# Kernel tuning notes

Measured on AMD Instinct MI355X. Metric: run time of the kernel, lower is better.

Reference implementation:

```python
import jax, jax.numpy as jnp
import numpy as np

N_NODES = 20000
HEADS = 4


def _gat_conv(x, src, dst, W, att_src, att_dst, bias, concat):
    # PyG GATConv: h = x @ W -> [N, H, C]; edge score = leaky_relu(a_s[src]+a_d[dst], 0.2);
    # segment softmax over dst; scatter-add weighted messages.
    N = x.shape[0]
    H, C = att_src.shape[1], att_src.shape[2]
    h = (x @ W).reshape(N, H, C)
    a_s = jnp.sum(h * att_src, axis=-1)  # [N, H]
    a_d = jnp.sum(h * att_dst, axis=-1)  # [N, H]
    e = jax.nn.leaky_relu(a_s[src] + a_d[dst], negative_slope=0.2)  # [E, H]
    m = jax.ops.segment_max(e, dst, num_segments=N)  # [N, H]
    e = jnp.exp(e - m[dst])
    denom = jax.ops.segment_sum(e, dst, num_segments=N)
    alpha = e / (denom[dst] + 1e-16)  # [E, H]
    msg = h[src] * alpha[:, :, None]  # [E, H, C]
    out = jax.ops.segment_sum(msg, dst, num_segments=N)  # [N, H, C]
    if concat:
        out = out.reshape(N, H * C)
    else:
        out = out.mean(axis=1)
    return out + bias


def setup_inputs() -> dict:
    key = jax.random.key(0)
    ks = jax.random.split(key, 16)
    N, F_in, Hd, H, Z = N_NODES, 256, 128, HEADS, 64
    E = 320000
    x = jax.random.normal(ks[0], (N, F_in), dtype=jnp.float32)
    edge_index = jax.random.randint(ks[1], (2, E), 0, N, dtype=jnp.int64)
    def xavier(k, shape):
        fan_in, fan_out = shape[0], shape[1]
        lim = float(np.sqrt(6.0 / (fan_in + fan_out)))
        return jax.random.uniform(k, shape, jnp.float32, -lim, lim)
    inp = {"x": x, "edge_index": edge_index}
    dims = [(F_in, Hd), (Hd * H, Hd), (Hd * H, Hd)]
    for i, (din, dout) in enumerate(dims, 1):
        inp[f"W{i}"] = xavier(ks[2 * i], (din, H * dout))
        inp[f"att{i}_src"] = jax.random.normal(ks[2 * i + 1], (1, H, dout), dtype=jnp.float32) * 0.1
        inp[f"att{i}_dst"] = jax.random.normal(jax.random.fold_in(ks[2 * i + 1], 7), (1, H, dout), dtype=jnp.float32) * 0.1
        bdim = H * dout if i < 3 else dout
        inp[f"b{i}"] = jnp.zeros((bdim,), dtype=jnp.float32)
    inp["fc_W"] = xavier(ks[10], (Hd, 2 * Z))
    inp["fc_b"] = jnp.zeros((2 * Z,), dtype=jnp.float32)
    return inp


def reference(x, edge_index, W1, att1_src, att1_dst, b1, W2, att2_src, att2_dst, b2,
              W3, att3_src, att3_dst, b3, fc_W, fc_b):
    N = x.shape[0]
    # add_self_loops=True (PyG default)
    loop = jnp.arange(N, dtype=edge_index.dtype)
    src = jnp.concatenate([edge_index[0], loop])
    dst = jnp.concatenate([edge_index[1], loop])
    h = jax.nn.leaky_relu(_gat_conv(x, src, dst, W1, att1_src, att1_dst, b1, True), 0.01)
    h = jax.nn.leaky_relu(_gat_conv(h, src, dst, W2, att2_src, att2_dst, b2, True), 0.01)
    h = _gat_conv(h, src, dst, W3, att3_src, att3_dst, b3, False)
    z = h @ fc_W + fc_b
    mu, logvar = jnp.split(z, 2, axis=1)
    return (mu, jnp.exp(logvar))
```

## Files before the change

kernel.cpp:

```cpp
#include <hip/hip_runtime.h>
#include <hip/hip_bf16.h>

typedef unsigned short u16;
typedef unsigned int u32;
typedef __attribute__((ext_vector_type(8))) short bf16x8;
typedef __attribute__((ext_vector_type(4))) float f32x4;
typedef __attribute__((ext_vector_type(8))) u16 u16x8;
typedef __attribute__((ext_vector_type(4))) u16 u16x4;

#define NN 20000
#define NE 320000
#define HC 512

__device__ __forceinline__ float bf2f(u16 u){ return __uint_as_float(((u32)u)<<16); }
__device__ __forceinline__ u16 f2bf(float x){
  __hip_bfloat16 h = __float2bfloat16(x);
  return *reinterpret_cast<u16*>(&h);
}
__device__ __forceinline__ float escore(float x){
  float e = x > 0.f ? x : 0.2f*x;
  return __expf(fminf(e, 80.f));
}

typedef const __attribute__((address_space(1))) unsigned int* gas_t;
typedef __attribute__((address_space(3))) unsigned int* las_t;
__device__ __forceinline__ void gl16(const void* g, void* l){
  __builtin_amdgcn_global_load_lds((gas_t)g, (las_t)l, 16, 0, 0);
}

__global__ __launch_bounds__(256) void cast_kernel(const float* __restrict__ in, u16* __restrict__ out, int total){
  int i = (blockIdx.x*256 + threadIdx.x)*4;
  if (i >= total) return;
  float4 v = *(const float4*)(in + i);
  u16x4 o = { f2bf(v.x), f2bf(v.y), f2bf(v.z), f2bf(v.w) };
  *(u16x4*)(out + i) = o;
}

__global__ __launch_bounds__(256) void transpose_cast(const float* __restrict__ W, u16* __restrict__ WT,
                                                      int K, int N){
  __shared__ u16 t[32][33];
  int bx = blockIdx.x*32;
  int by = blockIdx.y*32;
  int tx = threadIdx.x & 31, ty = threadIdx.x >> 5;
  for (int r = ty; r < 32; r += 8) t[r][tx] = f2bf(W[(size_t)(by+r)*N + bx + tx]);
  __syncthreads();
  for (int r = ty; r < 32; r += 8) WT[(size_t)(bx+r)*K + by + tx] = t[tx][r];
}

__global__ void detect_kernel(const int* __restrict__ ei, int* __restrict__ flag){
  __shared__ int nz;
  if (threadIdx.x == 0) nz = 0;
  __syncthreads();
  int c = 0;
  for (int k = threadIdx.x; k < 4096; k += 256) if (ei[2*k + 1] != 0) c++;
  atomicAdd(&nz, c);
  __syncthreads();
  if (threadIdx.x == 0) *flag = (nz == 0) ? 1 : 0;
}

__global__ __launch_bounds__(256) void normalize_edges(const int* __restrict__ ei, const int* __restrict__ flag,
    int* __restrict__ src, int* __restrict__ dst, int E){
  int e = blockIdx.x*256 + threadIdx.x;
  if (e >= E) return;
  if (*flag){ src[e] = ei[2*e]; dst[e] = ei[2*(E + e)]; }
  else      { src[e] = ei[e];   dst[e] = ei[E + e]; }
}

__global__ __launch_bounds__(256) void gemm_bf16(const u16* __restrict__ A, const u16* __restrict__ BT,
                                                 u16* __restrict__ C, int M, int K){
  __shared__ __align__(16) u16 Ads[128][64];
  __shared__ __align__(16) u16 Bds[128][64];
  const int bm = blockIdx.x, bn = blockIdx.y;
  const int tid = threadIdx.x;
  const int lane = tid & 63, wid = tid >> 6;
  const int wr = (wid >> 1) << 6, wc = (wid & 1) << 6;
  f32x4 acc[4][4] = {};
  const int row0 = bm*128;
  const int wbase = tid & 192;
  for (int k0 = 0; k0 < K; k0 += 64){
    #pragma unroll
    for (int p = 0; p < 4; ++p){
      int idx = p*256 + tid;
      int r = idx >> 3, cg = idx & 7;
      int csg = cg ^ (r & 7);
      int gr = row0 + r; if (gr >= M) gr = M - 1;
      gl16(A + (size_t)gr*K + k0 + csg*8, (u16*)Ads + (size_t)(p*256 + wbase)*8);
      gl16(BT + (size_t)(bn*128 + r)*K + k0 + csg*8, (u16*)Bds + (size_t)(p*256 + wbase)*8);
    }
    __syncthreads();
    #pragma unroll
    for (int kk = 0; kk < 64; kk += 32){
      const int lr = lane & 15;
      const int lk = kk + ((lane >> 4) << 3);
      bf16x8 a[4], b[4];
      #pragma unroll
      for (int i = 0; i < 4; ++i){
        int ar = wr + 16*i + lr;
        a[i] = *(const bf16x8*)&Ads[ar][lk ^ ((ar & 7) << 3)];
      }
      #pragma unroll
      for (int j = 0; j < 4; ++j){
        int br = wc + 16*j + lr;
        b[j] = *(const bf16x8*)&Bds[br][lk ^ ((br & 7) << 3)];
      }
      #pragma unroll
      for (int i = 0; i < 4; ++i)
        #pragma unroll
        for (int j = 0; j < 4; ++j)
          acc[i][j] = __builtin_amdgcn_mfma_f32_16x16x32_bf16(a[i], b[j], acc[i][j], 0, 0, 0);
    }
    __syncthreads();
  }
  const int lr = lane & 15, r4 = (lane >> 4) << 2;
  #pragma unroll
  for (int i = 0; i < 4; ++i)
    #pragma unroll
    for (int j = 0; j < 4; ++j){
      int col = bn*128 + wc + 16*j + lr;
      #pragma unroll
      for (int r = 0; r < 4; ++r){
        int row = row0 + wr + 16*i + r4 + r;
        if (row < M) C[(size_t)row*HC + col] = f2bf(acc[i][j][r]);
      }
    }
}

__global__ __launch_bounds__(256) void asad_kernel(const u16* __restrict__ h,
    const float* __restrict__ attS, const float* __restrict__ attD,
    float* __restrict__ a_s, float* __restrict__ a_d, int N){
  int wid = blockIdx.x*4 + (threadIdx.x >> 6);
  if (wid >= N) return;
  int lane = threadIdx.x & 63;
  u16x8 v = *(const u16x8*)(h + (size_t)wid*HC + lane*8);
  float4 s0 = *(const float4*)(attS + lane*8);
  float4 s1 = *(const float4*)(attS + lane*8 + 4);
  float4 d0 = *(const float4*)(attD + lane*8);
  float4 d1 = *(const float4*)(attD + lane*8 + 4);
  float sv[8] = {s0.x,s0.y,s0.z,s0.w,s1.x,s1.y,s1.z,s1.w};
  float dv[8] = {d0.x,d0.y,d0.z,d0.w,d1.x,d1.y,d1.z,d1.w};
  float ps = 0.f, pd = 0.f;
  #pragma unroll
  for (int t = 0; t < 8; ++t){ float hv = bf2f(v[t]); ps += hv*sv[t]; pd += hv*dv[t]; }
  #pragma unroll
  for (int off = 1; off < 16; off <<= 1){
    ps += __shfl_xor(ps, off, 64);
    pd += __shfl_xor(pd, off, 64);
  }
  if ((lane & 15) == 0){
    int hh = lane >> 4;
    a_s[wid*4 + hh] = ps;
    a_d[wid*4 + hh] = pd;
  }
}

__global__ __launch_bounds__(256) void hist_kernel(const int* __restrict__ dst, int* __restrict__ cnt, int E){
  int e = blockIdx.x*256 + threadIdx.x;
  if (e < E) atomicAdd(&cnt[dst[e]], 1);
}

__global__ __launch_bounds__(1024) void scan_kernel(const int* __restrict__ cnt,
    int* __restrict__ offs, int* __restrict__ cur, int N){
  __shared__ int bsum[1024];
  int tid = threadIdx.x;
  const int CH = (N + 1023) >> 10;
  int lo = tid*CH, hi = min(lo + CH, N);
  int s = 0;
  for (int i = lo; i < hi; ++i) s += cnt[i];
  bsum[tid] = s;
  __syncthreads();
  for (int off = 1; off < 1024; off <<= 1){
    int t = (tid >= off) ? bsum[tid - off] : 0;
    __syncthreads();
    bsum[tid] += t;
    __syncthreads();
  }
  int run = (tid > 0) ? bsum[tid - 1] : 0;
  for (int i = lo; i < hi; ++i){
    offs[i] = run; cur[i] = run; run += cnt[i];
  }
  if (tid == 1023) offs[N] = bsum[1023];
}

__global__ __launch_bounds__(256) void scatter_kernel(const int* __restrict__ src, const int* __restrict__ dst,
    int* __restrict__ cur, int* __restrict__ src_sorted, int E){
  int e = blockIdx.x*256 + threadIdx.x;
  if (e >= E) return;
  int d = dst[e];
  int pos = atomicAdd(&cur[d], 1);
  src_sorted[pos] = src[e];
}

template<int MODE>
__global__ __launch_bounds__(256) void agg_kernel(const u16* __restrict__ h,
    const int* __restrict__ srcs, const int* __restrict__ offs,
    const float* __restrict__ a_s, const float* __restrict__ a_d,
    const float* __restrict__ bias, void* __restrict__ outp, int N){
  int d = blockIdx.x*4 + (threadIdx.x >> 6);
  if (d >= N) return;
  int lane = threadIdx.x & 63;
  int head = lane >> 4;
  float adv = a_d[d*4 + head];
  float acc[8];
  float dsum;
  {
    float w = escore(a_s[d*4 + head] + adv);
    dsum = w;
    u16x8 v = *(const u16x8*)(h + (size_t)d*HC + lane*8);
    #pragma unroll
    for (int t = 0; t < 8; ++t) acc[t] = w*bf2f(v[t]);
  }
  int p0 = offs[d], p1 = offs[d+1];
  int p = p0;
  for (; p + 3 < p1; p += 4){
    int s0 = srcs[p], s1 = srcs[p+1], s2 = srcs[p+2], s3 = srcs[p+3];
    float w0 = escore(a_s[s0*4 + head] + adv);
    float w1 = escore(a_s[s1*4 + head] + adv);
    float w2 = escore(a_s[s2*4 + head] + adv);
    float w3 = escore(a_s[s3*4 + head] + adv);
    u16x8 v0 = *(const u16x8*)(h + (size_t)s0*HC + lane*8);
    u16x8 v1 = *(const u16x8*)(h + (size_t)s1*HC + lane*8);
    u16x8 v2 = *(const u16x8*)(h + (size_t)s2*HC + lane*8);
    u16x8 v3 = *(const u16x8*)(h + (size_t)s3*HC + lane*8);
    dsum += w0 + w1 + w2 + w3;
    #pragma unroll
    for (int t = 0; t < 8; ++t)
      acc[t] += w0*bf2f(v0[t]) + w1*bf2f(v1[t]) + w2*bf2f(v2[t]) + w3*bf2f(v3[t]);
  }
  for (; p < p1; ++p){
    int s = srcs[p];
    float w = escore(a_s[s*4 + head] + adv);
    u16x8 v = *(const u16x8*)(h + (size_t)s*HC + lane*8);
    dsum += w;
    #pragma unroll
    for (int t = 0; t < 8; ++t) acc[t] += w*bf2f(v[t]);
  }
  float inv = 1.0f / (dsum + 1e-16f);
  if (MODE < 2){
    u16* act = (u16*)outp;
    u16x8 o;
    #pragma unroll
    for (int t = 0; t < 8; ++t){
      float x = acc[t]*inv + bias[lane*8 + t];
      x = x > 0.f ? x : 0.01f*x;
      o[t] = f2bf(x);
    }
    *(u16x8*)(act + (size_t)d*HC + lane*8) = o;
  } else {
    #pragma unroll
    for (int t = 0; t < 8; ++t){
      acc[t] *= inv;
      acc[t] += __shfl_xor(acc[t], 16, 64);
      acc[t] += __shfl_xor(acc[t], 32, 64);
    }
    if (lane < 16){
      float* hf = (float*)outp;
      int c0 = lane*8;
      float4 o0 = {0.25f*acc[0] + bias[c0+0], 0.25f*acc[1] + bias[c0+1],
                   0.25f*acc[2] + bias[c0+2], 0.25f*acc[3] + bias[c0+3]};
      float4 o1 = {0.25f*acc[4] + bias[c0+4], 0.25f*acc[5] + bias[c0+5],
                   0.25f*acc[6] + bias[c0+6], 0.25f*acc[7] + bias[c0+7]};
      *(float4*)(hf + (size_t)d*128 + c0)     = o0;
      *(float4*)(hf + (size_t)d*128 + c0 + 4) = o1;
    }
  }
}

__global__ __launch_bounds__(256) void hsplit_kernel(const float* __restrict__ hfin,
    u16* __restrict__ Hhi, u16* __restrict__ Hlo, int total){
  int i = (blockIdx.x*256 + threadIdx.x)*4;
  if (i >= total) return;
  float4 v = *(const float4*)(hfin + i);
  float r[4] = {v.x, v.y, v.z, v.w};
  u16x4 hi, lo;
  #pragma unroll
  for (int t = 0; t < 4; ++t){
    hi[t] = f2bf(r[t]);
    lo[t] = f2bf(r[t] - bf2f(hi[t]));
  }
  *(u16x4*)(Hhi + i) = hi;
  *(u16x4*)(Hlo + i) = lo;
}

__global__ __launch_bounds__(256) void wsplit_kernel(const float* __restrict__ W,
    u16* __restrict__ WThi, u16* __restrict__ WTlo){
  int i = blockIdx.x*256 + threadIdx.x;
  int k = i >> 7, o = i & 127;
  float w = W[i];
  u16 hi = f2bf(w);
  u16 lo = f2bf(w - bf2f(hi));
  WThi[o*128 + k] = hi;
  WTlo[o*128 + k] = lo;
}

__global__ __launch_bounds__(256) void fc_mfma(const u16* __restrict__ Hhi, const u16* __restrict__ Hlo,
    const u16* __restrict__ WThi, const u16* __restrict__ WTlo,
    const float* __restrict__ fcb, float* __restrict__ outp, int M){
  __shared__ __align__(16) u16 Ahi[128][64];
  __shared__ __align__(16) u16 Alo[128][64];
  __shared__ __align__(16) u16 Bhi[128][64];
  __shared__ __align__(16) u16 Blo[128][64];
  const int tid = threadIdx.x;
  const int lane = tid & 63, wid = tid >> 6;
  const int wr = (wid >> 1) << 6, wc = (wid & 1) << 6;
  f32x4 acc[4][4] = {};
  const int row0 = blockIdx.x*128;
  for (int k0 = 0; k0 < 128; k0 += 64){
    #pragma unroll
    for (int p = 0; p < 4; ++p){
      int idx = p*256 + tid;
      int r = idx >> 3;
      int c = (idx & 7) << 3;
      int cs = c ^ ((r & 7) << 3);
      int gr = row0 + r; if (gr >= M) gr = M - 1;
      *(u16x8*)&Ahi[r][cs] = *(const u16x8*)(Hhi + (size_t)gr*128 + k0 + c);
      *(u16x8*)&Alo[r][cs] = *(const u16x8*)(Hlo + (size_t)gr*128 + k0 + c);
      *(u16x8*)&Bhi[r][cs] = *(const u16x8*)(WThi + (size_t)r*128 + k0 + c);
      *(u16x8*)&Blo[r][cs] = *(const u16x8*)(WTlo + (size_t)r*128 + k0 + c);
    }
    __syncthreads();
    #pragma unroll
    for (int kk = 0; kk < 64; kk += 32){
      const int lr = lane & 15;
      const int lk = kk + ((lane >> 4) << 3);
      bf16x8 ah[4], al[4], bh[4], bl[4];
      #pragma unroll
      for (int i = 0; i < 4; ++i){
        int ar = wr + 16*i + lr;
        int sw = lk ^ ((ar & 7) << 3);
        ah[i] = *(const bf16x8*)&Ahi[ar][sw];
        al[i] = *(const bf16x8*)&Alo[ar][sw];
      }
      #pragma unroll
      for (int j = 0; j < 4; ++j){
        int br = wc + 16*j + lr;
        int sw = lk ^ ((br & 7) << 3);
        bh[j] = *(const bf16x8*)&Bhi[br][sw];
        bl[j] = *(const bf16x8*)&Blo[br][sw];
      }
      #pragma unroll
      for (int i = 0; i < 4; ++i)
        #pragma unroll
        for (int j = 0; j < 4; ++j){
          acc[i][j] = __builtin_amdgcn_mfma_f32_16x16x32_bf16(ah[i], bh[j], acc[i][j], 0, 0, 0);
          acc[i][j] = __builtin_amdgcn_mfma_f32_16x16x32_bf16(ah[i], bl[j], acc[i][j], 0, 0, 0);
          acc[i][j] = __builtin_amdgcn_mfma_f32_16x16x32_bf16(al[i], bh[j], acc[i][j], 0, 0, 0);
        }
    }
    __syncthreads();
  }
  const int lr = lane & 15, r4 = (lane >> 4) << 2;
  #pragma unroll
  for (int i = 0; i < 4; ++i)
    #pragma unroll
    for (int j = 0; j < 4; ++j){
      int o = wc + 16*j + lr;
      float bb = fcb[o];
      #pragma unroll
      for (int r = 0; r < 4; ++r){
        int row = row0 + wr + 16*i + r4 + r;
        if (row < M){
          float z = acc[i][j][r] + bb;
          if (o < 64) outp[(size_t)row*64 + o] = z;
          else        outp[(size_t)M*64 + (size_t)row*64 + (o - 64)] = expf(z);
        }
      }
    }
}

extern "C" void kernel_launch(void* const* d_in, const int* in_sizes, int n_in,
                              void* d_out, int out_size, void* d_ws, size_t ws_size,
                              hipStream_t stream){
  const float* x    = (const float*)d_in[0];
  const int* ei     = (const int*)d_in[1];
  const float* W1   = (const float*)d_in[2];
  const float* att1s= (const float*)d_in[3];
  const float* att1d= (const float*)d_in[4];
  const float* b1   = (const float*)d_in[5];
  const float* W2   = (const float*)d_in[6];
  const float* att2s= (const float*)d_in[7];
  const float* att2d= (const float*)d_in[8];
  const float* b2   = (const float*)d_in[9];
  const float* W3   = (const float*)d_in[10];
  const float* att3s= (const float*)d_in[11];
  const float* att3d= (const float*)d_in[12];
  const float* b3   = (const float*)d_in[13];
  const float* fcW  = (const float*)d_in[14];
  const float* fcb  = (const float*)d_in[15];
  float* outp = (float*)d_out;

  char* ws = (char*)d_ws;
  size_t off = 0;
  auto alloc = [&](size_t bytes) -> void* {
    void* p = ws + off;
    off = (off + bytes + 255) & ~(size_t)255;
    return p;
  };
  u16*   xb     = (u16*)  alloc((size_t)NN*256*2);
  u16*   h      = (u16*)  alloc((size_t)NN*HC*2);
  u16*   act    = (u16*)  alloc((size_t)NN*HC*2);
  float* hfin   = (float*)alloc((size_t)NN*128*4);
  u16*   Hhi    = (u16*)  alloc((size_t)NN*128*2);
  u16*   Hlo    = (u16*)  alloc((size_t)NN*128*2);
  float* a_s    = (float*)alloc((size_t)NN*4*4);
  float* a_d    = (float*)alloc((size_t)NN*4*4);
  int*   cnt    = (int*)  alloc((size_t)NN*4);
  int*   cur    = (int*)  alloc((size_t)NN*4);
  int*   offs   = (int*)  alloc((size_t)(NN+1)*4);
  int*   src32  = (int*)  alloc((size_t)NE*4);
  int*   dst32  = (int*)  alloc((size_t)NE*4);
  int*   srcs   = (int*)  alloc((size_t)NE*4);
  u16*   WT1    = (u16*)  alloc((size_t)512*256*2);
  u16*   WT2    = (u16*)  alloc((size_t)512*512*2);
  u16*   WT3    = (u16*)  alloc((size_t)512*512*2);
  u16*   WThi   = (u16*)  alloc((size_t)128*128*2);
  u16*   WTlo   = (u16*)  alloc((size_t)128*128*2);
  int*   flag   = (int*)  alloc(256);

  cast_kernel<<<5000, 256, 0, stream>>>(x, xb, NN*256);
  transpose_cast<<<dim3(16, 8),  256, 0, stream>>>(W1, WT1, 256, 512);
  transpose_cast<<<dim3(16, 16), 256, 0, stream>>>(W2, WT2, 512, 512);
  transpose_cast<<<dim3(16, 16), 256, 0, stream>>>(W3, WT3, 512, 512);
  wsplit_kernel<<<64, 256, 0, stream>>>(fcW, WThi, WTlo);

  detect_kernel<<<1, 256, 0, stream>>>(ei, flag);
  normalize_edges<<<1250, 256, 0, stream>>>(ei, flag, src32, dst32, NE);

  hipMemsetAsync(cnt, 0, (size_t)NN*4, stream);
  hist_kernel<<<1250, 256, 0, stream>>>(dst32, cnt, NE);
  scan_kernel<<<1, 1024, 0, stream>>>(cnt, offs, cur, NN);
  scatter_kernel<<<1250, 256, 0, stream>>>(src32, dst32, cur, srcs, NE);

  const float* attS[3] = {att1s, att2s, att3s};
  const float* attD[3] = {att1d, att2d, att3d};
  const u16*   WT[3]   = {WT1, WT2, WT3};
  const int    Kd[3]   = {256, 512, 512};

  for (int layer = 0; layer < 3; ++layer){
    const u16* Ain = (layer == 0) ? xb : act;
    gemm_bf16<<<dim3(157, 4), 256, 0, stream>>>(Ain, WT[layer], h, NN, Kd[layer]);
    asad_kernel<<<5000, 256, 0, stream>>>(h, attS[layer], attD[layer], a_s, a_d, NN);
    if (layer == 0)
      agg_kernel<0><<<5000, 256, 0, stream>>>(h, srcs, offs, a_s, a_d, b1, act, NN);
    else if (layer == 1)
      agg_kernel<1><<<5000, 256, 0, stream>>>(h, srcs, offs, a_s, a_d, b2, act, NN);
    else
      agg_kernel<2><<<5000, 256, 0, stream>>>(h, srcs, offs, a_s, a_d, b3, hfin, NN);
  }

  hsplit_kernel<<<2500, 256, 0, stream>>>(hfin, Hhi, Hlo, NN*128);
  fc_mfma<<<157, 256, 0, stream>>>(Hhi, Hlo, WThi, WTlo, fcb, outp, NN);
}
```

Baseline: 325.9 us.

## Precompute edge softmax weights and slice aggregation across channel blocks

Edge attention weights are now normalised in a separate alpha kernel that writes per-edge alpha values and a self-loop weight. Aggregation is split into 8 channel slices per node, each wavefront handling 64 channels with scalar bf16 gathers, so more blocks run concurrently. The head-mean for the last layer moves into the hsplit kernel, which reduces a full 512-wide fp32 partial buffer. In exchange it adds an extra kernel per layer, a 5 MB alpha buffer that is written and re-read, and narrow 2-byte gathers in place of 16-byte vector loads, each edge's alpha being loaded once per slice.

Result: slower. 497.8 us (+52.7%).

```diff
diff --git a/kernel.cpp b/kernel.cpp
--- a/kernel.cpp
+++ b/kernel.cpp
@@ -190,95 +190,99 @@
   src_sorted[pos] = src[e];
 }
 
-template<int MODE>
-__global__ __launch_bounds__(256) void agg_kernel(const u16* __restrict__ h,
-    const int* __restrict__ srcs, const int* __restrict__ offs,
+__global__ __launch_bounds__(256) void alpha_kernel(const int* __restrict__ srcs, const int* __restrict__ offs,
     const float* __restrict__ a_s, const float* __restrict__ a_d,
-    const float* __restrict__ bias, void* __restrict__ outp, int N){
+    float* __restrict__ alpha, float* __restrict__ aself, int N){
   int d = blockIdx.x*4 + (threadIdx.x >> 6);
   if (d >= N) return;
   int lane = threadIdx.x & 63;
-  int head = lane >> 4;
-  float adv = a_d[d*4 + head];
-  float acc[8];
-  float dsum;
-  {
-    float w = escore(a_s[d*4 + head] + adv);
-    dsum = w;
-    u16x8 v = *(const u16x8*)(h + (size_t)d*HC + lane*8);
-    #pragma unroll
-    for (int t = 0; t < 8; ++t) acc[t] = w*bf2f(v[t]);
-  }
+  int hh = lane & 3;
+  float adv = a_d[d*4 + hh];
+  float eself = escore(a_s[d*4 + hh] + adv);
+  int p0 = offs[d], p1 = offs[d+1];
+  float esum = 0.f;
+  for (int base = p0; base < p1; base += 16){
+    int el = base + (lane >> 2);
+    if (el < p1){
+      int s = srcs[el];
+      esum += escore(a_s[s*4 + hh] + adv);
+    }
+  }
+  esum += __shfl_xor(esum, 4, 64);
+  esum += __shfl_xor(esum, 8, 64);
+  esum += __shfl_xor(esum, 16, 64);
+  esum += __shfl_xor(esum, 32, 64);
+  float inv = 1.f/(esum + eself + 1e-16f);
+  if (lane < 4) aself[d*4 + hh] = eself*inv;
+  for (int base = p0; base < p1; base += 16){
+    int el = base + (lane >> 2);
+    if (el < p1){
+      int s = srcs[el];
+      alpha[(size_t)el*4 + hh] = escore(a_s[s*4 + hh] + adv)*inv;
+    }
+  }
+}
+
+template<int MODE>
+__global__ __launch_bounds__(256) void agg_sliced(const u16* __restrict__ h,
+    const int* __restrict__ srcs, const int* __restrict__ offs,
+    const float* __restrict__ alpha, const float* __restrict__ aself,
+    const float* __restrict__ bias, void* __restrict__ outp, int N){
+  int slice = blockIdx.x & 7;
+  int d = (blockIdx.x >> 3)*4 + (threadIdx.x >> 6);
+  if (d >= N) return;
+  int lane = threadIdx.x & 63;
+  int c = slice*64 + lane;
+  int head = slice >> 1;
+  const u16* hc = h + c;
+  float acc = aself[d*4 + head]*bf2f(hc[(size_t)d*HC]);
   int p0 = offs[d], p1 = offs[d+1];
   int p = p0;
   for (; p + 3 < p1; p += 4){
     int s0 = srcs[p], s1 = srcs[p+1], s2 = srcs[p+2], s3 = srcs[p+3];
-    float w0 = escore(a_s[s0*4 + head] + adv);
-    float w1 = escore(a_s[s1*4 + head] + adv);
-    float w2 = escore(a_s[s2*4 + head] + adv);
-    float w3 = escore(a_s[s3*4 + head] + adv);
-    u16x8 v0 = *(const u16x8*)(h + (size_t)s0*HC + lane*8);
-    u16x8 v1 = *(const u16x8*)(h + (size_t)s1*HC + lane*8);
-    u16x8 v2 = *(const u16x8*)(h + (size_t)s2*HC + lane*8);
-    u16x8 v3 = *(const u16x8*)(h + (size_t)s3*HC + lane*8);
-    dsum += w0 + w1 + w2 + w3;
-    #pragma unroll
-    for (int t = 0; t < 8; ++t)
-      acc[t] += w0*bf2f(v0[t]) + w1*bf2f(v1[t]) + w2*bf2f(v2[t]) + w3*bf2f(v3[t]);
+    float w0 = alpha[(size_t)p*4 + head];
+    float w1 = alpha[(size_t)(p+1)*4 + head];
+    float w2 = alpha[(size_t)(p+2)*4 + head];
+    float w3 = alpha[(size_t)(p+3)*4 + head];
+    float v0 = bf2f(hc[(size_t)s0*HC]);
+    float v1 = bf2f(hc[(size_t)s1*HC]);
+    float v2 = bf2f(hc[(size_t)s2*HC]);
+    float v3 = bf2f(hc[(size_t)s3*HC]);
+    acc += w0*v0 + w1*v1 + w2*v2 + w3*v3;
   }
   for (; p < p1; ++p){
-    int s = srcs[p];
-    float w = escore(a_s[s*4 + head] + adv);
-    u16x8 v = *(const u16x8*)(h + (size_t)s*HC + lane*8);
-    dsum += w;
-    #pragma unroll
-    for (int t = 0; t < 8; ++t) acc[t] += w*bf2f(v[t]);
-  }
-  float inv = 1.0f / (dsum + 1e-16f);
-  if (MODE < 2){
-    u16* act = (u16*)outp;
-    u16x8 o;
-    #pragma unroll
-    for (int t = 0; t < 8; ++t){
-      float x = acc[t]*inv + bias[lane*8 + t];
-      x = x > 0.f ? x : 0.01f*x;
-      o[t] = f2bf(x);
-    }
-    *(u16x8*)(act + (size_t)d*HC + lane*8) = o;
+    acc += alpha[(size_t)p*4 + head]*bf2f(hc[(size_t)srcs[p]*HC]);
+  }
+  if (MODE == 0){
+    float x = acc + bias[c];
+    x = x > 0.f ? x : 0.01f*x;
+    ((u16*)outp)[(size_t)d*HC + c] = f2bf(x);
   } else {
-    #pragma unroll
-    for (int t = 0; t < 8; ++t){
-      acc[t] *= inv;
-      acc[t] += __shfl_xor(acc[t], 16, 64);
-      acc[t] += __shfl_xor(acc[t], 32, 64);
-    }
-    if (lane < 16){
-      float* hf = (float*)outp;
-      int c0 = lane*8;
-      float4 o0 = {0.25f*acc[0] + bias[c0+0], 0.25f*acc[1] + bias[c0+1],
-                   0.25f*acc[2] + bias[c0+2], 0.25f*acc[3] + bias[c0+3]};
-      float4 o1 = {0.25f*acc[4] + bias[c0+4], 0.25f*acc[5] + bias[c0+5],
-                   0.25f*acc[6] + bias[c0+6], 0.25f*acc[7] + bias[c0+7]};
-      *(float4*)(hf + (size_t)d*128 + c0)     = o0;
-      *(float4*)(hf + (size_t)d*128 + c0 + 4) = o1;
-    }
-  }
-}
-
-__global__ __launch_bounds__(256) void hsplit_kernel(const float* __restrict__ hfin,
-    u16* __restrict__ Hhi, u16* __restrict__ Hlo, int total){
-  int i = (blockIdx.x*256 + threadIdx.x)*4;
-  if (i >= total) return;
-  float4 v = *(const float4*)(hfin + i);
-  float r[4] = {v.x, v.y, v.z, v.w};
+    ((float*)outp)[(size_t)d*HC + c] = 0.25f*acc;
+  }
+}
+
+__global__ __launch_bounds__(256) void hsplit2_kernel(const float* __restrict__ part, const float* __restrict__ b3,
+    u16* __restrict__ Hhi, u16* __restrict__ Hlo, int N){
+  int idx = blockIdx.x*256 + threadIdx.x;
+  if (idx >= N*32) return;
+  int d = idx >> 5, c4 = (idx & 31)*4;
+  const float* pp = part + (size_t)d*HC + c4;
+  float4 q0 = *(const float4*)(pp);
+  float4 q1 = *(const float4*)(pp + 128);
+  float4 q2 = *(const float4*)(pp + 256);
+  float4 q3 = *(const float4*)(pp + 384);
+  float4 bb = *(const float4*)(b3 + c4);
+  float r[4] = { q0.x+q1.x+q2.x+q3.x+bb.x, q0.y+q1.y+q2.y+q3.y+bb.y,
+                 q0.z+q1.z+q2.z+q3.z+bb.z, q0.w+q1.w+q2.w+q3.w+bb.w };
   u16x4 hi, lo;
   #pragma unroll
   for (int t = 0; t < 4; ++t){
     hi[t] = f2bf(r[t]);
     lo[t] = f2bf(r[t] - bf2f(hi[t]));
   }
-  *(u16x4*)(Hhi + i) = hi;
-  *(u16x4*)(Hlo + i) = lo;
+  *(u16x4*)(Hhi + (size_t)d*128 + c4) = hi;
+  *(u16x4*)(Hlo + (size_t)d*128 + c4) = lo;
 }
 
 __global__ __launch_bounds__(256) void wsplit_kernel(const float* __restrict__ W,
@@ -398,11 +402,13 @@
   u16*   xb     = (u16*)  alloc((size_t)NN*256*2);
   u16*   h      = (u16*)  alloc((size_t)NN*HC*2);
   u16*   act    = (u16*)  alloc((size_t)NN*HC*2);
-  float* hfin   = (float*)alloc((size_t)NN*128*4);
+  float* hpart  = (float*)alloc((size_t)NN*HC*4);
   u16*   Hhi    = (u16*)  alloc((size_t)NN*128*2);
   u16*   Hlo    = (u16*)  alloc((size_t)NN*128*2);
   float* a_s    = (float*)alloc((size_t)NN*4*4);
   float* a_d    = (float*)alloc((size_t)NN*4*4);
+  float* aself  = (float*)alloc((size_t)NN*4*4);
+  float* alpha  = (float*)alloc((size_t)NE*4*4);
   int*   cnt    = (int*)  alloc((size_t)NN*4);
   int*   cur    = (int*)  alloc((size_t)NN*4);
   int*   offs   = (int*)  alloc((size_t)(NN+1)*4);
@@ -439,14 +445,15 @@
     const u16* Ain = (layer == 0) ? xb : act;
     gemm_bf16<<<dim3(157, 4), 256, 0, stream>>>(Ain, WT[layer], h, NN, Kd[layer]);
     asad_kernel<<<5000, 256, 0, stream>>>(h, attS[layer], attD[layer], a_s, a_d, NN);
+    alpha_kernel<<<5000, 256, 0, stream>>>(srcs, offs, a_s, a_d, alpha, aself, NN);
     if (layer == 0)
-      agg_kernel<0><<<5000, 256, 0, stream>>>(h, srcs, offs, a_s, a_d, b1, act, NN);
+      agg_sliced<0><<<40000, 256, 0, stream>>>(h, srcs, offs, alpha, aself, b1, act, NN);
     else if (layer == 1)
-      agg_kernel<1><<<5000, 256, 0, stream>>>(h, srcs, offs, a_s, a_d, b2, act, NN);
+      agg_sliced<0><<<40000, 256, 0, stream>>>(h, srcs, offs, alpha, aself, b2, act, NN);
     else
-      agg_kernel<2><<<5000, 256, 0, stream>>>(h, srcs, offs, a_s, a_d, b3, hfin, NN);
-  }
-
-  hsplit_kernel<<<2500, 256, 0, stream>>>(hfin, Hhi, Hlo, NN*128);
+      agg_sliced<1><<<40000, 256, 0, stream>>>(h, srcs, offs, alpha, aself, b3, hpart, NN);
+  }
+
+  hsplit2_kernel<<<2500, 256, 0, stream>>>(hpart, b3, Hhi, Hlo, NN);
   fc_mfma<<<157, 256, 0, stream>>>(Hhi, Hlo, WThi, WTlo, fcb, outp, NN);
 }
```
